# Performance work log

Hardware: AMD Instinct MI355X
Metric: run time of the kernel (lower is better)

The kernel has to match this reference:

```python
import math
import jax, jax.numpy as jnp
import numpy as np

N_NODES = 10000
N_EDGES = 160000
F_IN = 256
HID = 500
N_OUT = 100


def setup_inputs() -> dict:
    key = jax.random.key(0)
    ks = jax.random.split(key, 20)
    inp = {}
    inp['x'] = jax.random.normal(ks[0], (N_NODES, F_IN), jnp.float32)
    inp['edge_src'] = jax.random.randint(ks[1], (N_EDGES,), 0, N_NODES, jnp.int32)
    inp['edge_dst'] = jax.random.randint(ks[2], (N_EDGES,), 0, N_NODES, jnp.int32)
    inp['edge_weight'] = jax.random.uniform(ks[3], (N_EDGES,), jnp.float32)
    s1 = 1.0 / math.sqrt(F_IN)
    s2 = 1.0 / math.sqrt(HID)
    inp['W1_rel'] = jax.random.uniform(ks[4], (HID, F_IN), jnp.float32, -s1, s1)
    inp['b1'] = jax.random.uniform(ks[5], (HID,), jnp.float32, -s1, s1)
    inp['W1_root'] = jax.random.uniform(ks[6], (HID, F_IN), jnp.float32, -s1, s1)
    inp['p1_w'] = jax.random.uniform(ks[7], (HID,), jnp.float32, -s2, s2)
    inp['W2_rel'] = jax.random.uniform(ks[8], (HID, HID), jnp.float32, -s2, s2)
    inp['b2'] = jax.random.uniform(ks[9], (HID,), jnp.float32, -s2, s2)
    inp['W2_root'] = jax.random.uniform(ks[10], (HID, HID), jnp.float32, -s2, s2)
    inp['p2_w'] = jax.random.uniform(ks[11], (HID,), jnp.float32, -s2, s2)
    s3 = 1.0 / math.sqrt(1000)
    inp['lin1_W'] = jax.random.uniform(ks[12], (2000, 1000), jnp.float32, -s3, s3)
    inp['lin1_b'] = jax.random.uniform(ks[13], (2000,), jnp.float32, -s3, s3)
    s4 = 1.0 / math.sqrt(2000)
    inp['lin2_W'] = jax.random.uniform(ks[14], (4000, 2000), jnp.float32, -s4, s4)
    inp['lin2_b'] = jax.random.uniform(ks[15], (4000,), jnp.float32, -s4, s4)
    s5 = 1.0 / math.sqrt(4000)
    inp['lin3_W'] = jax.random.uniform(ks[16], (N_OUT, 4000), jnp.float32, -s5, s5)
    inp['lin3_b'] = jax.random.uniform(ks[17], (N_OUT,), jnp.float32, -s5, s5)
    return inp


def graph_conv(x, src, dst, w, W_rel, b_rel, W_root):
    # PyG GraphConv: out_i = W_rel @ sum_{j->i} w_ji * x_j + b + W_root @ x_i
    msg = x[src] * w[:, None]                              # [E, F]
    agg = jax.ops.segment_sum(msg, dst, num_segments=x.shape[0])
    return agg @ W_rel.T + b_rel + x @ W_root.T


def topk_pool(x, src, dst, w, p_w, ratio=0.5):
    # PyG TopKPooling: score = tanh(x @ p / ||p||); keep top-k; scale x by score.
    N = x.shape[0]
    k = int(math.ceil(ratio * N))
    score = jnp.tanh((x @ p_w) / jnp.linalg.norm(p_w))
    vals, perm = jax.lax.top_k(score, k)
    x_new = x[perm] * vals[:, None]
    # keep fixed-size edge list; dropped edges get weight 0 and point to node 0
    new_idx = jnp.zeros((N,), jnp.int32).at[perm].set(jnp.arange(k, dtype=jnp.int32))
    mask = jnp.zeros((N,), bool).at[perm].set(True)
    keep = mask[src] & mask[dst]
    src_new = jnp.where(keep, new_idx[src], 0)
    dst_new = jnp.where(keep, new_idx[dst], 0)
    w_new = jnp.where(keep, w, 0.0)
    return x_new, src_new, dst_new, w_new


def readout(x):
    # global max pool + global mean pool over the single graph -> [1, 2F]
    return jnp.concatenate([jnp.max(x, 0, keepdims=True), jnp.mean(x, 0, keepdims=True)], axis=1)


def reference(x, edge_src, edge_dst, edge_weight,
              W1_rel, b1, W1_root, p1_w,
              W2_rel, b2, W2_root, p2_w,
              lin1_W, lin1_b, lin2_W, lin2_b, lin3_W, lin3_b):
    h = jax.nn.relu(graph_conv(x, edge_src, edge_dst, edge_weight, W1_rel, b1, W1_root))
    h, s1, d1, w1 = topk_pool(h, edge_src, edge_dst, edge_weight, p1_w)
    x1 = readout(h)
    h = jax.nn.relu(graph_conv(h, s1, d1, w1, W2_rel, b2, W2_root))
    h, _, _, _ = topk_pool(h, s1, d1, w1, p2_w)
    x2 = readout(h)
    z = x1 + x2                                            # [1, 1000]
    z = jax.nn.relu(z @ lin1_W.T + lin1_b)
    z = jax.nn.relu(z @ lin2_W.T + lin2_b)                 # dropout is identity at eval
    return jax.nn.sigmoid(z @ lin3_W.T + lin3_b)
```

## Files before the change

kernel.cpp:

```cpp
#include <hip/hip_runtime.h>
#include <hip/hip_bf16.h>
#include <math.h>

#define NN1   10000
#define NE    160000
#define FIN   256
#define HID   500
#define K1    5000
#define NN2   5000
#define K2    2500

#define CSR_OFFS   0u
#define CSR_POS    10008u
#define CSR_EDGE   20008u
#define OFF_AGG    340016u
#define OFF_H      2900016u
#define OFF_XP2    (OFF_H + 2500000u)
#define OFF_SCP    7900016u
#define OFF_RK1    10410016u
#define OFF_Z      10432016u
#define OFF_T1     10433016u
#define OFF_T2     10435016u
#define OFF_INV    10439016u
#define OFF_CNT    10439024u
#define OFF_PM1    10639024u
#define OFF_PS1    10671024u
#define OFF_XB     10703024u
#define OFF_W1RB   11983024u
#define OFF_W1TB   12047024u
#define OFF_W2RB   12111024u
#define OFF_W2TB   12236024u
#define OFF_XP1B   12361024u
#define OFF_PM2    13611024u
#define OFF_PS2    13627024u
#define WS_FLOATS  13643024u

#define RCHUNK 500
#define ROSLAB1 64
#define ROSLAB2 32
#define RORPB   79

__device__ inline unsigned f2ord(float f) {
    unsigned u = __float_as_uint(f);
    return (u & 0x80000000u) ? ~u : (u | 0x80000000u);
}
__device__ inline unsigned long long rkey(float s, int j) {
    return ((unsigned long long)f2ord(s) << 32) | (unsigned)(0xFFFFFFFFu - (unsigned)j);
}
__device__ inline unsigned short bf16rn(float f) {
    unsigned u = __float_as_uint(f);
    u += 0x7FFFu + ((u >> 16) & 1u);
    return (unsigned short)(u >> 16);
}
__device__ inline float bf2f(unsigned short u) {
    return __uint_as_float((unsigned)u << 16);
}

typedef __attribute__((ext_vector_type(8))) short short8;
typedef __attribute__((ext_vector_type(4))) float floatx4;


__global__ __launch_bounds__(256) void k_prep(
    const float* __restrict__ x, unsigned short* __restrict__ xb,
    const float* __restrict__ w1r, unsigned short* __restrict__ w1rb,
    const float* __restrict__ w1t, unsigned short* __restrict__ w1tb,
    const float* __restrict__ w2r, unsigned short* __restrict__ w2rb,
    const float* __restrict__ w2t, unsigned short* __restrict__ w2tb,
    const float* __restrict__ p1, const float* __restrict__ p2,
    float* __restrict__ invn,
    const int* __restrict__ edst, int* __restrict__ pos) {
    __shared__ float red[256];
    int y = blockIdx.y;
    if (y < 5) {
        const float* s; unsigned short* d; int n;
        switch (y) {
            case 0: s = x;   d = xb;   n = NN1 * FIN; break;
            case 1: s = w1r; d = w1rb; n = HID * FIN; break;
            case 2: s = w1t; d = w1tb; n = HID * FIN; break;
            case 3: s = w2r; d = w2rb; n = HID * HID; break;
            default: s = w2t; d = w2tb; n = HID * HID; break;
        }
        int i = (blockIdx.x * 256 + threadIdx.x) * 4;
        if (i >= n) return;
        if (i + 3 < n) {
            float4 v = *(const float4*)(s + i);
            ushort4 o;
            o.x = bf16rn(v.x); o.y = bf16rn(v.y); o.z = bf16rn(v.z); o.w = bf16rn(v.w);
            *(ushort4*)(d + i) = o;
        } else {
            for (int q = 0; q < 4 && i + q < n; ++q) d[i + q] = bf16rn(s[i + q]);
        }
    } else if (y == 5) {
        if (blockIdx.x >= 2) return;
        const float* p = blockIdx.x ? p2 : p1;
        float s = 0.f;
        for (int i = threadIdx.x; i < HID; i += 256) { float v = p[i]; s += v * v; }
        red[threadIdx.x] = s; __syncthreads();
        for (int w = 128; w > 0; w >>= 1) {
            if (threadIdx.x < w) red[threadIdx.x] += red[threadIdx.x + w];
            __syncthreads();
        }
        if (threadIdx.x == 0) invn[blockIdx.x] = 1.0f / sqrtf(red[0]);
    } else {
        int e = blockIdx.x * 256 + threadIdx.x;
        if (e < NE) atomicAdd(&pos[edst[e]], 1);
    }
}

__global__ __launch_bounds__(1024) void k_scan(int* __restrict__ pos, int* __restrict__ offs) {
    __shared__ int tot[1024];
    int t = threadIdx.x;
    int base = t * 10;
    int loc[10]; int s = 0;
    #pragma unroll
    for (int q = 0; q < 10; ++q) {
        int v = (base + q < NN1) ? pos[base + q] : 0;
        loc[q] = s; s += v;
    }
    tot[t] = s; __syncthreads();
    for (int d = 1; d < 1024; d <<= 1) {
        int v = (t >= d) ? tot[t - d] : 0;
        __syncthreads();
        tot[t] += v;
        __syncthreads();
    }
    int excl = (t == 0) ? 0 : tot[t - 1];
    #pragma unroll
    for (int q = 0; q < 10; ++q)
        if (base + q < NN1) { int o = excl + loc[q]; offs[base + q] = o; pos[base + q] = o; }
    if (t == 1023) offs[NN1] = tot[1023];
}

__global__ void k_fill(const int* __restrict__ src, const int* __restrict__ dst,
                       const float* __restrict__ w, int* __restrict__ pos,
                       int2* __restrict__ ce) {
    int e = blockIdx.x * 256 + threadIdx.x;
    if (e >= NE) return;
    int slot = atomicAdd(&pos[dst[e]], 1);
    ce[slot] = make_int2(src[e], __float_as_int(w[e]));
}

__global__ __launch_bounds__(256) void k_gather1(
    const unsigned short* __restrict__ xb, const int* __restrict__ offs,
    const int2* __restrict__ ce, unsigned short* __restrict__ aggb) {
    int wave = (blockIdx.x * 256 + threadIdx.x) >> 6;
    int lane = threadIdx.x & 63;
    if (wave >= NN1) return;
    int b = offs[wave], e = offs[wave + 1];
    float4 a0 = make_float4(0.f, 0.f, 0.f, 0.f);
    float4 a1 = make_float4(0.f, 0.f, 0.f, 0.f);
    int p = b;
    for (; p + 1 < e; p += 2) {
        int2 e0 = ce[p], e1 = ce[p + 1];
        float w0 = __int_as_float(e0.y), w1 = __int_as_float(e1.y);
        ushort4 u0 = *(const ushort4*)(xb + (size_t)e0.x * FIN + lane * 4);
        ushort4 u1 = *(const ushort4*)(xb + (size_t)e1.x * FIN + lane * 4);
        a0.x += bf2f(u0.x) * w0; a0.y += bf2f(u0.y) * w0;
        a0.z += bf2f(u0.z) * w0; a0.w += bf2f(u0.w) * w0;
        a1.x += bf2f(u1.x) * w1; a1.y += bf2f(u1.y) * w1;
        a1.z += bf2f(u1.z) * w1; a1.w += bf2f(u1.w) * w1;
    }
    if (p < e) {
        int2 e0 = ce[p];
        float w0 = __int_as_float(e0.y);
        ushort4 u0 = *(const ushort4*)(xb + (size_t)e0.x * FIN + lane * 4);
        a0.x += bf2f(u0.x) * w0; a0.y += bf2f(u0.y) * w0;
        a0.z += bf2f(u0.z) * w0; a0.w += bf2f(u0.w) * w0;
    }
    ushort4 o;
    o.x = bf16rn(a0.x + a1.x); o.y = bf16rn(a0.y + a1.y);
    o.z = bf16rn(a0.z + a1.z); o.w = bf16rn(a0.w + a1.w);
    *(ushort4*)(aggb + (size_t)wave * FIN + lane * 4) = o;
}

__global__ __launch_bounds__(256) void k_gather2(
    const unsigned short* __restrict__ Xb, const int* __restrict__ offs,
    const int2* __restrict__ ce, const int* __restrict__ rank,
    unsigned short* __restrict__ aggb) {
    int wave = (blockIdx.x * 256 + threadIdx.x) >> 6;
    int lane = threadIdx.x & 63;
    if (wave >= NN1) return;
    int rd = rank[wave];
    if (rd < 0) return;
    int b = offs[wave], e = offs[wave + 1];
    int c1 = 256 + lane * 4;
    float a0 = 0.f, a1 = 0.f, a2 = 0.f, a3 = 0.f;
    float b0 = 0.f, b1v = 0.f, b2 = 0.f, b3 = 0.f;
    int2 nxt = (b < e) ? ce[b] : make_int2(0, 0);
    for (int p = b; p < e; ++p) {
        int2 cur = nxt;
        if (p + 1 < e) nxt = ce[p + 1];
        int rs = rank[cur.x];
        if (rs < 0) continue;
        float we = __int_as_float(cur.y);
        const unsigned short* row = Xb + (size_t)rs * HID;
        ushort4 u = *(const ushort4*)(row + lane * 4);
        a0 += bf2f(u.x) * we; a1 += bf2f(u.y) * we;
        a2 += bf2f(u.z) * we; a3 += bf2f(u.w) * we;
        if (c1 < HID) {
            ushort4 u2 = *(const ushort4*)(row + c1);
            b0 += bf2f(u2.x) * we; b1v += bf2f(u2.y) * we;
            b2 += bf2f(u2.z) * we; b3 += bf2f(u2.w) * we;
        }
    }
    unsigned short* o = aggb + (size_t)rd * HID;
    ushort4 o1; o1.x = bf16rn(a0); o1.y = bf16rn(a1); o1.z = bf16rn(a2); o1.w = bf16rn(a3);
    *(ushort4*)(o + lane * 4) = o1;
    if (c1 < HID) {
        ushort4 o2; o2.x = bf16rn(b0); o2.y = bf16rn(b1v); o2.z = bf16rn(b2); o2.w = bf16rn(b3);
        *(ushort4*)(o + c1) = o2;
    }
}

__device__ inline short8 ld8g(const unsigned short* p, int gk, int K) {
    if (gk + 7 < K) return *(const short8*)p;
    unsigned short tmp[8] = {0,0,0,0,0,0,0,0};
    for (int q = 0; q < 8; ++q) if (gk + q < K) tmp[q] = p[q];
    return *(short8*)tmp;
}

#define GBK 64
__global__ __launch_bounds__(256) void k_gemm_bf16(
    const unsigned short* __restrict__ A1, const unsigned short* __restrict__ B1,
    const unsigned short* __restrict__ A2, const unsigned short* __restrict__ B2,
    const float* __restrict__ bias, const float* __restrict__ pv,
    unsigned short* __restrict__ C, float* __restrict__ scpart,
    int M, int N, int Ka, int Kb, int nbyRow) {
    int b = blockIdx.x;
    int xcd = b & 7, seq = b >> 3;
    int colT = seq & 7;
    int rowT = xcd + 8 * (seq >> 3);
    if (rowT >= nbyRow) return;
    int row0 = rowT * 64, col0 = colT * 64;

    __shared__ unsigned short As[2][64 * 64];
    __shared__ unsigned short Bs[2][64 * 64];
    int tid = threadIdx.x;
    int lane = tid & 63, wid = tid >> 6;
    int waveM = wid & 1, waveN = wid >> 1;
    int quad = lane >> 4, mrow = lane & 15;
    int m7 = mrow & 7;
    floatx4 acc[2][2] = {};

    int sr = tid >> 2;
    int ca = (tid & 3) * 2;
    int s7 = sr & 7;
    int c0 = (ca ^ s7) * 8;
    int c1 = ((ca + 1) ^ s7) * 8;
    int sbase = sr * 64;

    int nka = (Ka + GBK - 1) / GBK;
    int nkb = (Kb + GBK - 1) / GBK;
    int niter = nka + nkb;

    short8 z8 = {0,0,0,0,0,0,0,0};
    short8 paA = z8, paB = z8, pbA = z8, pbB = z8;

    auto fetch = [&](int t) {
        int ph = (t >= nka);
        const unsigned short* A = ph ? A2 : A1;
        const unsigned short* B = ph ? B2 : B1;
        int K = ph ? Kb : Ka;
        int gk = (ph ? t - nka : t) * GBK + ca * 8;
        int gr = row0 + sr, gn = col0 + sr;
        paA = z8; paB = z8; pbA = z8; pbB = z8;
        if (gr < M) {
            const unsigned short* p = A + (size_t)gr * K + gk;
            paA = ld8g(p, gk, K); paB = ld8g(p + 8, gk + 8, K);
        }
        if (gn < N) {
            const unsigned short* p = B + (size_t)gn * K + gk;
            pbA = ld8g(p, gk, K); pbB = ld8g(p + 8, gk + 8, K);
        }
    };
    auto commit = [&](int buf) {
        *(short8*)&As[buf][sbase + c0] = paA;
        *(short8*)&As[buf][sbase + c1] = paB;
        *(short8*)&Bs[buf][sbase + c0] = pbA;
        *(short8*)&Bs[buf][sbase + c1] = pbB;
    };

    fetch(0);
    commit(0);
    if (niter > 1) fetch(1);
    __syncthreads();

    for (int it = 0; it < niter; ++it) {
        int cur = it & 1;
        if (it + 1 < niter) commit(cur ^ 1);
        if (it + 2 < niter) fetch(it + 2);
        #pragma unroll
        for (int half = 0; half < 2; ++half) {
            int qc = half * 4 + quad;
            int qoff = (qc ^ m7) * 8;
            short8 bfr[2];
            #pragma unroll
            for (int nt = 0; nt < 2; ++nt)
                bfr[nt] = *(short8*)&Bs[cur][(waveN * 32 + nt * 16 + mrow) * 64 + qoff];
            #pragma unroll
            for (int mt = 0; mt < 2; ++mt) {
                short8 afr = *(short8*)&As[cur][(waveM * 32 + mt * 16 + mrow) * 64 + qoff];
                #pragma unroll
                for (int nt = 0; nt < 2; ++nt)
                    acc[mt][nt] = __builtin_amdgcn_mfma_f32_16x16x32_bf16(
                        afr, bfr[nt], acc[mt][nt], 0, 0, 0);
            }
        }
        __syncthreads();
    }
    float ps[2][4] = {};
    #pragma unroll
    for (int nt = 0; nt < 2; ++nt) {
        int col = col0 + waveN * 32 + nt * 16 + mrow;
        if (col >= N) continue;
        float bv = bias[col];
        float pc = pv[col];
        #pragma unroll
        for (int mt = 0; mt < 2; ++mt) {
            int rbase = row0 + waveM * 32 + mt * 16 + quad * 4;
            #pragma unroll
            for (int r = 0; r < 4; ++r) {
                float v = fmaxf(acc[mt][nt][r] + bv, 0.f);
                int row = rbase + r;
                if (row < M) C[(size_t)row * N + col] = bf16rn(v);
                ps[mt][r] += v * pc;
            }
        }
    }
    int part = colT * 2 + waveN;
    #pragma unroll
    for (int mt = 0; mt < 2; ++mt)
        #pragma unroll
        for (int r = 0; r < 4; ++r) {
            float v = ps[mt][r];
            v += __shfl_xor(v, 1, 64); v += __shfl_xor(v, 2, 64);
            v += __shfl_xor(v, 4, 64); v += __shfl_xor(v, 8, 64);
            if (mrow == 0) {
                int row = row0 + waveM * 32 + mt * 16 + quad * 4 + r;
                if (row < M) scpart[(size_t)part * M + row] = v;
            }
        }
}

__global__ __launch_bounds__(256) void k_rank_partial(
    const float* __restrict__ scpart, int* __restrict__ cntp, int Nn) {
    __shared__ unsigned long long kj[RCHUNK];
    int j0 = blockIdx.y * RCHUNK;
    int jn = min(Nn - j0, RCHUNK);
    for (int t = threadIdx.x; t < jn; t += 256) {
        float s = 0.f;
        #pragma unroll
        for (int q = 0; q < 16; ++q) s += scpart[(size_t)q * Nn + j0 + t];
        kj[t] = rkey(s, j0 + t);
    }
    __syncthreads();
    int i = blockIdx.x * 256 + threadIdx.x;
    if (i >= Nn) return;
    float si = 0.f;
    #pragma unroll
    for (int q = 0; q < 16; ++q) si += scpart[(size_t)q * Nn + i];
    unsigned long long ki = rkey(si, i);
    int c = 0;
    #pragma unroll 4
    for (int q = 0; q < jn; ++q)
        c += (kj[q] > ki) ? 1 : 0;
    cntp[(size_t)blockIdx.y * Nn + i] = c;
}

__global__ __launch_bounds__(128) void k_gather_pool(
    const unsigned short* __restrict__ Hb, const float* __restrict__ scpart,
    const float* __restrict__ invn,
    const int* __restrict__ cntp, int Nn, int nchunk, int kk,
    int* __restrict__ rank_out, unsigned short* __restrict__ Xb) {
    __shared__ int csum[128];
    __shared__ float ssum[128];
    __shared__ int rsh;
    __shared__ float scsh;
    int i = blockIdx.x;
    int c = 0;
    for (int q = threadIdx.x; q < nchunk; q += 128) c += cntp[(size_t)q * Nn + i];
    float s = (threadIdx.x < 16) ? scpart[(size_t)threadIdx.x * Nn + i] : 0.f;
    csum[threadIdx.x] = c; ssum[threadIdx.x] = s;
    __syncthreads();
    if (threadIdx.x == 0) {
        int t = 0;
        int lim = (nchunk < 128) ? nchunk : 128;
        for (int q = 0; q < lim; ++q) t += csum[q];
        float st = 0.f;
        for (int q = 0; q < 16; ++q) st += ssum[q];
        int r = (t < kk) ? t : -1;
        if (rank_out) rank_out[i] = r;
        rsh = r;
        scsh = tanhf(st * invn[0]);
    }
    __syncthreads();
    int r = rsh;
    if (r < 0) return;
    float sc = scsh;
    int cc = threadIdx.x;
    if (cc < HID / 4) {
        ushort4 u = *(const ushort4*)(Hb + (size_t)i * HID + cc * 4);
        ushort4 o;
        o.x = bf16rn(bf2f(u.x) * sc); o.y = bf16rn(bf2f(u.y) * sc);
        o.z = bf16rn(bf2f(u.z) * sc); o.w = bf16rn(bf2f(u.w) * sc);
        *(ushort4*)(Xb + (size_t)r * HID + cc * 4) = o;
    }
}

__global__ __launch_bounds__(256) void k_readout_slab(
    const unsigned short* __restrict__ X, int rows, int rpb,
    float* __restrict__ pmax, float* __restrict__ psum) {
    __shared__ float4 lmx[4][64];
    __shared__ float4 lsm[4][64];
    int lane = threadIdx.x & 63;
    int rgrp = threadIdx.x >> 6;
    int c4 = blockIdx.x * 64 + lane;
    int r0 = blockIdx.y * rpb;
    int r1 = min(rows, r0 + rpb);
    float4 mx = make_float4(-INFINITY, -INFINITY, -INFINITY, -INFINITY);
    float4 sm = make_float4(0.f, 0.f, 0.f, 0.f);
    if (c4 < HID / 4) {
        for (int r = r0 + rgrp; r < r1; r += 4) {
            ushort4 u = *(const ushort4*)(X + (size_t)r * HID + c4 * 4);
            float vx = bf2f(u.x), vy = bf2f(u.y), vz = bf2f(u.z), vw = bf2f(u.w);
            mx.x = fmaxf(mx.x, vx); mx.y = fmaxf(mx.y, vy);
            mx.z = fmaxf(mx.z, vz); mx.w = fmaxf(mx.w, vw);
            sm.x += vx; sm.y += vy; sm.z += vz; sm.w += vw;
        }
    }
    lmx[rgrp][lane] = mx; lsm[rgrp][lane] = sm;
    __syncthreads();
    if (rgrp == 0 && c4 < HID / 4) {
        #pragma unroll
        for (int g = 1; g < 4; ++g) {
            float4 m2 = lmx[g][lane], s2 = lsm[g][lane];
            mx.x = fmaxf(mx.x, m2.x); mx.y = fmaxf(mx.y, m2.y);
            mx.z = fmaxf(mx.z, m2.z); mx.w = fmaxf(mx.w, m2.w);
            sm.x += s2.x; sm.y += s2.y; sm.z += s2.z; sm.w += s2.w;
        }
        *(float4*)(pmax + (size_t)blockIdx.y * HID + c4 * 4) = mx;
        *(float4*)(psum + (size_t)blockIdx.y * HID + c4 * 4) = sm;
    }
}

__global__ __launch_bounds__(64) void k_combine_all(
    const float* __restrict__ pm1, const float* __restrict__ ps1, int ns1,
    const float* __restrict__ pm2, const float* __restrict__ ps2, int ns2,
    float* __restrict__ z) {
    int j = blockIdx.x * 64 + threadIdx.x;
    if (j >= HID) return;
    float m1 = -INFINITY, s1 = 0.f;
    for (int s = 0; s < ns1; ++s) {
        m1 = fmaxf(m1, pm1[(size_t)s * HID + j]);
        s1 += ps1[(size_t)s * HID + j];
    }
    float m2 = -INFINITY, s2 = 0.f;
    for (int s = 0; s < ns2; ++s) {
        m2 = fmaxf(m2, pm2[(size_t)s * HID + j]);
        s2 += ps2[(size_t)s * HID + j];
    }
    z[j] = m1 + m2;
    z[HID + j] = s1 * (1.0f / (float)K1) + s2 * (1.0f / (float)K2);
}

__global__ __launch_bounds__(256) void k_mv(
    const float* __restrict__ v, const float* __restrict__ W,
    const float* __restrict__ bias, float* __restrict__ y,
    int rowsN, int K, int act) {
    int wave = (blockIdx.x * 256 + threadIdx.x) >> 6;
    int lane = threadIdx.x & 63;
    if (wave >= rowsN) return;
    const float* wr = W + (size_t)wave * K;
    float s = 0.f;
    for (int c = lane * 4; c < K; c += 256) {
        float4 a = *(const float4*)(wr + c);
        float4 xv = *(const float4*)(v + c);
        s += a.x * xv.x + a.y * xv.y + a.z * xv.z + a.w * xv.w;
    }
    for (int off = 32; off > 0; off >>= 1) s += __shfl_down(s, off, 64);
    if (lane == 0) {
        float r = s + bias[wave];
        y[wave] = (act == 0) ? fmaxf(r, 0.f) : 1.f / (1.f + expf(-r));
    }
}

extern "C" void kernel_launch(void* const* d_in, const int* in_sizes, int n_in,
                              void* d_out, int out_size, void* d_ws, size_t ws_size,
                              hipStream_t stream) {
    const float* x      = (const float*)d_in[0];
    const int*   esrc   = (const int*)d_in[1];
    const int*   edst   = (const int*)d_in[2];
    const float* ew     = (const float*)d_in[3];
    const float* W1_rel = (const float*)d_in[4];
    const float* b1     = (const float*)d_in[5];
    const float* W1_root= (const float*)d_in[6];
    const float* p1     = (const float*)d_in[7];
    const float* W2_rel = (const float*)d_in[8];
    const float* b2     = (const float*)d_in[9];
    const float* W2_root= (const float*)d_in[10];
    const float* p2     = (const float*)d_in[11];
    const float* l1W    = (const float*)d_in[12];
    const float* l1b    = (const float*)d_in[13];
    const float* l2W    = (const float*)d_in[14];
    const float* l2b    = (const float*)d_in[15];
    const float* l3W    = (const float*)d_in[16];
    const float* l3b    = (const float*)d_in[17];
    float* out = (float*)d_out;
    float* ws  = (float*)d_ws;

    if (ws_size < (size_t)WS_FLOATS * sizeof(float)) return;

    int*            offs  = (int*)(ws + CSR_OFFS);
    int*            pos   = (int*)(ws + CSR_POS);
    int2*           ce    = (int2*)(ws + CSR_EDGE);
    unsigned short* aggb  = (unsigned short*)(ws + OFF_AGG);
    unsigned short* hb    = (unsigned short*)(ws + OFF_H);
    unsigned short* xp2b  = (unsigned short*)(ws + OFF_XP2);
    float*          scp   = ws + OFF_SCP;
    int*            rk1   = (int*)(ws + OFF_RK1);
    float*          zbuf  = ws + OFF_Z;
    float*          t1    = ws + OFF_T1;
    float*          t2    = ws + OFF_T2;
    float*          invn  = ws + OFF_INV;
    int*            cntp  = (int*)(ws + OFF_CNT);
    float*          pm1   = ws + OFF_PM1;
    float*          ps1   = ws + OFF_PS1;
    float*          pm2   = ws + OFF_PM2;
    float*          ps2   = ws + OFF_PS2;
    unsigned short* xb    = (unsigned short*)(ws + OFF_XB);
    unsigned short* w1rb  = (unsigned short*)(ws + OFF_W1RB);
    unsigned short* w1tb  = (unsigned short*)(ws + OFF_W1TB);
    unsigned short* w2rb  = (unsigned short*)(ws + OFF_W2RB);
    unsigned short* w2tb  = (unsigned short*)(ws + OFF_W2TB);
    unsigned short* xp1b  = (unsigned short*)(ws + OFF_XP1B);

    hipMemsetAsync(pos, 0, NN1 * sizeof(int), stream);
    k_prep<<<dim3(2500, 7), 256, 0, stream>>>(
        x, xb, W1_rel, w1rb, W1_root, w1tb, W2_rel, w2rb, W2_root, w2tb,
        p1, p2, invn, edst, pos);
    k_scan<<<1, 1024, 0, stream>>>(pos, offs);
    k_fill<<<(NE + 255) / 256, 256, 0, stream>>>(esrc, edst, ew, pos, ce);

    k_gather1<<<(NN1 * 64 + 255) / 256, 256, 0, stream>>>(xb, offs, ce, aggb);
    {
        int nby = (NN1 + 63) / 64;
        int nblk = 64 * ((nby + 7) / 8);
        k_gemm_bf16<<<nblk, 256, 0, stream>>>(
            aggb, w1rb, xb, w1tb, b1, p1, hb, scp, NN1, HID, FIN, FIN, nby);
    }

    k_rank_partial<<<dim3((NN1 + 255) / 256, NN1 / RCHUNK), 256, 0, stream>>>(scp, cntp, NN1);
    k_gather_pool<<<NN1, 128, 0, stream>>>(hb, scp, invn + 0, cntp, NN1, NN1 / RCHUNK, K1,
                                           rk1, xp1b);
    k_readout_slab<<<dim3(2, ROSLAB1), 256, 0, stream>>>(xp1b, K1, RORPB, pm1, ps1);

    k_gather2<<<(NN1 * 64 + 255) / 256, 256, 0, stream>>>(xp1b, offs, ce, rk1, aggb);
    {
        int nby = (NN2 + 63) / 64;
        int nblk = 64 * ((nby + 7) / 8);
        k_gemm_bf16<<<nblk, 256, 0, stream>>>(
            aggb, w2rb, xp1b, w2tb, b2, p2, hb, scp, NN2, HID, HID, HID, nby);
    }

    k_rank_partial<<<dim3((NN2 + 255) / 256, NN2 / RCHUNK), 256, 0, stream>>>(scp, cntp, NN2);
    k_gather_pool<<<NN2, 128, 0, stream>>>(hb, scp, invn + 1, cntp, NN2, NN2 / RCHUNK, K2,
                                           (int*)nullptr, xp2b);
    k_readout_slab<<<dim3(2, ROSLAB2), 256, 0, stream>>>(xp2b, K2, RORPB, pm2, ps2);
    k_combine_all<<<(HID + 63) / 64, 64, 0, stream>>>(pm1, ps1, ROSLAB1, pm2, ps2, ROSLAB2, zbuf);

    k_mv<<<(2000 * 64) / 256, 256, 0, stream>>>(zbuf, l1W, l1b, t1, 2000, 1000, 0);
    k_mv<<<(4000 * 64) / 256, 256, 0, stream>>>(t1, l2W, l2b, t2, 4000, 2000, 0);
    k_mv<<<(100 * 64) / 256, 256, 0, stream>>>(t2, l3W, l3b, out, 100, 4000, 1);
}
```

Before: 328.5 us.

## Precompute score keys once, widen rank chunks, wave-per-row pooling, flatten prep grid

A new kernel sums the per-partition score partials once and stores both the score and the sortable 64-bit key. The rank kernel then loads precomputed keys instead of summing 16 partials for every chunk and every node. The rank chunk doubles to 1000, which cuts the number of partial counts. The pooling gather now handles one row per 64-lane wave with a shuffle reduction instead of one row per 128-thread block with shared-memory syncs. The prep launch becomes a flat 1D grid so no idle blocks are launched for the small segments. The cost is one extra kernel launch per pooling stage.

```diff
diff --git a/kernel.cpp b/kernel.cpp
--- a/kernel.cpp
+++ b/kernel.cpp
@@ -17,6 +17,8 @@
 #define OFF_H      2900016u
 #define OFF_XP2    (OFF_H + 2500000u)
 #define OFF_SCP    7900016u
+#define OFF_KEY    8100016u
+#define OFF_SC     8150016u
 #define OFF_RK1    10410016u
 #define OFF_Z      10432016u
 #define OFF_T1     10433016u
@@ -35,10 +37,18 @@
 #define OFF_PS2    13627024u
 #define WS_FLOATS  13643024u
 
-#define RCHUNK 500
+#define RCHUNK 1000
 #define ROSLAB1 64
 #define ROSLAB2 32
 #define RORPB   79
+
+#define PB_S1 2500
+#define PB_S2 2625
+#define PB_S3 2750
+#define PB_S4 2995
+#define PB_S5 3240
+#define PB_S6 3242
+#define PB_S7 3867
 
 __device__ inline unsigned f2ord(float f) {
     unsigned u = __float_as_uint(f);
@@ -70,17 +80,15 @@
     float* __restrict__ invn,
     const int* __restrict__ edst, int* __restrict__ pos) {
     __shared__ float red[256];
-    int y = blockIdx.y;
-    if (y < 5) {
-        const float* s; unsigned short* d; int n;
-        switch (y) {
-            case 0: s = x;   d = xb;   n = NN1 * FIN; break;
-            case 1: s = w1r; d = w1rb; n = HID * FIN; break;
-            case 2: s = w1t; d = w1tb; n = HID * FIN; break;
-            case 3: s = w2r; d = w2rb; n = HID * HID; break;
-            default: s = w2t; d = w2tb; n = HID * HID; break;
-        }
-        int i = (blockIdx.x * 256 + threadIdx.x) * 4;
+    int b = blockIdx.x;
+    if (b < PB_S5) {
+        const float* s; unsigned short* d; int n; int lb;
+        if (b < PB_S1)      { s = x;   d = xb;   n = NN1 * FIN; lb = b; }
+        else if (b < PB_S2) { s = w1r; d = w1rb; n = HID * FIN; lb = b - PB_S1; }
+        else if (b < PB_S3) { s = w1t; d = w1tb; n = HID * FIN; lb = b - PB_S2; }
+        else if (b < PB_S4) { s = w2r; d = w2rb; n = HID * HID; lb = b - PB_S3; }
+        else                { s = w2t; d = w2tb; n = HID * HID; lb = b - PB_S4; }
+        int i = (lb * 256 + threadIdx.x) * 4;
         if (i >= n) return;
         if (i + 3 < n) {
             float4 v = *(const float4*)(s + i);
@@ -90,9 +98,8 @@
         } else {
             for (int q = 0; q < 4 && i + q < n; ++q) d[i + q] = bf16rn(s[i + q]);
         }
-    } else if (y == 5) {
-        if (blockIdx.x >= 2) return;
-        const float* p = blockIdx.x ? p2 : p1;
+    } else if (b < PB_S6) {
+        const float* p = (b - PB_S5) ? p2 : p1;
         float s = 0.f;
         for (int i = threadIdx.x; i < HID; i += 256) { float v = p[i]; s += v * v; }
         red[threadIdx.x] = s; __syncthreads();
@@ -100,9 +107,9 @@
             if (threadIdx.x < w) red[threadIdx.x] += red[threadIdx.x + w];
             __syncthreads();
         }
-        if (threadIdx.x == 0) invn[blockIdx.x] = 1.0f / sqrtf(red[0]);
+        if (threadIdx.x == 0) invn[b - PB_S5] = 1.0f / sqrtf(red[0]);
     } else {
-        int e = blockIdx.x * 256 + threadIdx.x;
+        int e = (b - PB_S6) * 256 + threadIdx.x;
         if (e < NE) atomicAdd(&pos[edst[e]], 1);
     }
 }
@@ -342,24 +349,29 @@
         }
 }
 
+__global__ __launch_bounds__(256) void k_scsum(
+    const float* __restrict__ scpart, float* __restrict__ sc,
+    unsigned long long* __restrict__ key, int Nn) {
+    int i = blockIdx.x * 256 + threadIdx.x;
+    if (i >= Nn) return;
+    float s = 0.f;
+    #pragma unroll
+    for (int q = 0; q < 16; ++q) s += scpart[(size_t)q * Nn + i];
+    sc[i] = s;
+    key[i] = rkey(s, i);
+}
+
 __global__ __launch_bounds__(256) void k_rank_partial(
-    const float* __restrict__ scpart, int* __restrict__ cntp, int Nn) {
+    const unsigned long long* __restrict__ key, int* __restrict__ cntp, int Nn) {
     __shared__ unsigned long long kj[RCHUNK];
     int j0 = blockIdx.y * RCHUNK;
     int jn = min(Nn - j0, RCHUNK);
-    for (int t = threadIdx.x; t < jn; t += 256) {
-        float s = 0.f;
-        #pragma unroll
-        for (int q = 0; q < 16; ++q) s += scpart[(size_t)q * Nn + j0 + t];
-        kj[t] = rkey(s, j0 + t);
-    }
+    for (int t = threadIdx.x; t < jn; t += 256)
+        kj[t] = key[j0 + t];
     __syncthreads();
     int i = blockIdx.x * 256 + threadIdx.x;
     if (i >= Nn) return;
-    float si = 0.f;
-    #pragma unroll
-    for (int q = 0; q < 16; ++q) si += scpart[(size_t)q * Nn + i];
-    unsigned long long ki = rkey(si, i);
+    unsigned long long ki = key[i];
     int c = 0;
     #pragma unroll 4
     for (int q = 0; q < jn; ++q)
@@ -367,42 +379,28 @@
     cntp[(size_t)blockIdx.y * Nn + i] = c;
 }
 
-__global__ __launch_bounds__(128) void k_gather_pool(
-    const unsigned short* __restrict__ Hb, const float* __restrict__ scpart,
+__global__ __launch_bounds__(256) void k_gather_pool(
+    const unsigned short* __restrict__ Hb, const float* __restrict__ sc,
     const float* __restrict__ invn,
     const int* __restrict__ cntp, int Nn, int nchunk, int kk,
     int* __restrict__ rank_out, unsigned short* __restrict__ Xb) {
-    __shared__ int csum[128];
-    __shared__ float ssum[128];
-    __shared__ int rsh;
-    __shared__ float scsh;
-    int i = blockIdx.x;
-    int c = 0;
-    for (int q = threadIdx.x; q < nchunk; q += 128) c += cntp[(size_t)q * Nn + i];
-    float s = (threadIdx.x < 16) ? scpart[(size_t)threadIdx.x * Nn + i] : 0.f;
-    csum[threadIdx.x] = c; ssum[threadIdx.x] = s;
-    __syncthreads();
-    if (threadIdx.x == 0) {
-        int t = 0;
-        int lim = (nchunk < 128) ? nchunk : 128;
-        for (int q = 0; q < lim; ++q) t += csum[q];
-        float st = 0.f;
-        for (int q = 0; q < 16; ++q) st += ssum[q];
-        int r = (t < kk) ? t : -1;
-        if (rank_out) rank_out[i] = r;
-        rsh = r;
-        scsh = tanhf(st * invn[0]);
-    }
-    __syncthreads();
-    int r = rsh;
+    int wave = (blockIdx.x * 256 + threadIdx.x) >> 6;
+    int lane = threadIdx.x & 63;
+    if (wave >= Nn) return;
+    int i = wave;
+    int c = (lane < nchunk) ? cntp[(size_t)lane * Nn + i] : 0;
+    #pragma unroll
+    for (int off = 8; off > 0; off >>= 1) c += __shfl_down(c, off, 64);
+    c = __shfl(c, 0, 64);
+    int r = (c < kk) ? c : -1;
+    if (lane == 0 && rank_out) rank_out[i] = r;
     if (r < 0) return;
-    float sc = scsh;
-    int cc = threadIdx.x;
-    if (cc < HID / 4) {
+    float s = tanhf(sc[i] * invn[0]);
+    for (int cc = lane; cc < HID / 4; cc += 64) {
         ushort4 u = *(const ushort4*)(Hb + (size_t)i * HID + cc * 4);
         ushort4 o;
-        o.x = bf16rn(bf2f(u.x) * sc); o.y = bf16rn(bf2f(u.y) * sc);
-        o.z = bf16rn(bf2f(u.z) * sc); o.w = bf16rn(bf2f(u.w) * sc);
+        o.x = bf16rn(bf2f(u.x) * s); o.y = bf16rn(bf2f(u.y) * s);
+        o.z = bf16rn(bf2f(u.z) * s); o.w = bf16rn(bf2f(u.w) * s);
         *(ushort4*)(Xb + (size_t)r * HID + cc * 4) = o;
     }
 }
@@ -510,32 +508,34 @@
 
     if (ws_size < (size_t)WS_FLOATS * sizeof(float)) return;
 
-    int*            offs  = (int*)(ws + CSR_OFFS);
-    int*            pos   = (int*)(ws + CSR_POS);
-    int2*           ce    = (int2*)(ws + CSR_EDGE);
-    unsigned short* aggb  = (unsigned short*)(ws + OFF_AGG);
-    unsigned short* hb    = (unsigned short*)(ws + OFF_H);
-    unsigned short* xp2b  = (unsigned short*)(ws + OFF_XP2);
-    float*          scp   = ws + OFF_SCP;
-    int*            rk1   = (int*)(ws + OFF_RK1);
-    float*          zbuf  = ws + OFF_Z;
-    float*          t1    = ws + OFF_T1;
-    float*          t2    = ws + OFF_T2;
-    float*          invn  = ws + OFF_INV;
-    int*            cntp  = (int*)(ws + OFF_CNT);
-    float*          pm1   = ws + OFF_PM1;
-    float*          ps1   = ws + OFF_PS1;
-    float*          pm2   = ws + OFF_PM2;
-    float*          ps2   = ws + OFF_PS2;
-    unsigned short* xb    = (unsigned short*)(ws + OFF_XB);
-    unsigned short* w1rb  = (unsigned short*)(ws + OFF_W1RB);
-    unsigned short* w1tb  = (unsigned short*)(ws + OFF_W1TB);
-    unsigned short* w2rb  = (unsigned short*)(ws + OFF_W2RB);
-    unsigned short* w2tb  = (unsigned short*)(ws + OFF_W2TB);
-    unsigned short* xp1b  = (unsigned short*)(ws + OFF_XP1B);
+    int*                offs  = (int*)(ws + CSR_OFFS);
+    int*                pos   = (int*)(ws + CSR_POS);
+    int2*               ce    = (int2*)(ws + CSR_EDGE);
+    unsigned short*     aggb  = (unsigned short*)(ws + OFF_AGG);
+    unsigned short*     hb    = (unsigned short*)(ws + OFF_H);
+    unsigned short*     xp2b  = (unsigned short*)(ws + OFF_XP2);
+    float*              scp   = ws + OFF_SCP;
+    unsigned long long* key   = (unsigned long long*)(ws + OFF_KEY);
+    float*              sc    = ws + OFF_SC;
+    int*                rk1   = (int*)(ws + OFF_RK1);
+    float*              zbuf  = ws + OFF_Z;
+    float*              t1    = ws + OFF_T1;
+    float*              t2    = ws + OFF_T2;
+    float*              invn  = ws + OFF_INV;
+    int*                cntp  = (int*)(ws + OFF_CNT);
+    float*              pm1   = ws + OFF_PM1;
+    float*              ps1   = ws + OFF_PS1;
+    float*              pm2   = ws + OFF_PM2;
+    float*              ps2   = ws + OFF_PS2;
+    unsigned short*     xb    = (unsigned short*)(ws + OFF_XB);
+    unsigned short*     w1rb  = (unsigned short*)(ws + OFF_W1RB);
+    unsigned short*     w1tb  = (unsigned short*)(ws + OFF_W1TB);
+    unsigned short*     w2rb  = (unsigned short*)(ws + OFF_W2RB);
+    unsigned short*     w2tb  = (unsigned short*)(ws + OFF_W2TB);
+    unsigned short*     xp1b  = (unsigned short*)(ws + OFF_XP1B);
 
     hipMemsetAsync(pos, 0, NN1 * sizeof(int), stream);
-    k_prep<<<dim3(2500, 7), 256, 0, stream>>>(
+    k_prep<<<PB_S7, 256, 0, stream>>>(
         x, xb, W1_rel, w1rb, W1_root, w1tb, W2_rel, w2rb, W2_root, w2tb,
         p1, p2, invn, edst, pos);
     k_scan<<<1, 1024, 0, stream>>>(pos, offs);
@@ -549,9 +549,10 @@
             aggb, w1rb, xb, w1tb, b1, p1, hb, scp, NN1, HID, FIN, FIN, nby);
     }
 
-    k_rank_partial<<<dim3((NN1 + 255) / 256, NN1 / RCHUNK), 256, 0, stream>>>(scp, cntp, NN1);
-    k_gather_pool<<<NN1, 128, 0, stream>>>(hb, scp, invn + 0, cntp, NN1, NN1 / RCHUNK, K1,
-                                           rk1, xp1b);
+    k_scsum<<<(NN1 + 255) / 256, 256, 0, stream>>>(scp, sc, key, NN1);
+    k_rank_partial<<<dim3((NN1 + 255) / 256, NN1 / RCHUNK), 256, 0, stream>>>(key, cntp, NN1);
+    k_gather_pool<<<(NN1 * 64 + 255) / 256, 256, 0, stream>>>(
+        hb, sc, invn + 0, cntp, NN1, NN1 / RCHUNK, K1, rk1, xp1b);
     k_readout_slab<<<dim3(2, ROSLAB1), 256, 0, stream>>>(xp1b, K1, RORPB, pm1, ps1);
 
     k_gather2<<<(NN1 * 64 + 255) / 256, 256, 0, stream>>>(xp1b, offs, ce, rk1, aggb);
@@ -562,9 +563,10 @@
             aggb, w2rb, xp1b, w2tb, b2, p2, hb, scp, NN2, HID, HID, HID, nby);
     }
 
-    k_rank_partial<<<dim3((NN2 + 255) / 256, NN2 / RCHUNK), 256, 0, stream>>>(scp, cntp, NN2);
-    k_gather_pool<<<NN2, 128, 0, stream>>>(hb, scp, invn + 1, cntp, NN2, NN2 / RCHUNK, K2,
-                                           (int*)nullptr, xp2b);
+    k_scsum<<<(NN2 + 255) / 256, 256, 0, stream>>>(scp, sc, key, NN2);
+    k_rank_partial<<<dim3((NN2 + 255) / 256, NN2 / RCHUNK), 256, 0, stream>>>(key, cntp, NN2);
+    k_gather_pool<<<(NN2 * 64 + 255) / 256, 256, 0, stream>>>(
+        hb, sc, invn + 1, cntp, NN2, NN2 / RCHUNK, K2, (int*)nullptr, xp2b);
     k_readout_slab<<<dim3(2, ROSLAB2), 256, 0, stream>>>(xp2b, K2, RORPB, pm2, ps2);
     k_combine_all<<<(HID + 63) / 64, 64, 0, stream>>>(pm1, ps1, ROSLAB1, pm2, ps2, ROSLAB2, zbuf);
 
```

After: 343.4 us. +4.6%, slower.
